# Optimization experiments

Hardware: AMD Instinct MI355X
Metric: run time of the kernel (lower is better)

Reference implementation:

```python
import jax, jax.numpy as jnp
import numpy as np


def setup_inputs() -> dict:
    key = jax.random.key(0)
    k1, k2, k3, k4, k5, k6, k7 = jax.random.split(key, 7)
    B, N, E = 8, 8192, 65536
    Dn, De = 64, 64            # node_shape, edge_shape
    IU = 128                   # input_units
    Dc = 2 * Dn + De           # concat dim = 192
    nodes = jax.random.normal(k1, (B, N, Dn), dtype=jnp.float32)
    edges = jax.random.normal(k2, (B, E, De), dtype=jnp.float32)
    senders = jax.random.randint(k3, (B, E), 0, N, dtype=jnp.int32)
    receivers = jax.random.randint(k4, (B, E), 0, N, dtype=jnp.int32)
    s_in = 1.0 / np.sqrt(Dc)
    s_out = 1.0 / np.sqrt(IU)
    s_edge = 1.0 / np.sqrt(Dn)
    W_in = jax.random.uniform(k5, (Dc, IU), jnp.float32, -s_in, s_in)
    b_in = jnp.zeros((IU,), jnp.float32)
    W_out = jax.random.uniform(k6, (IU, Dn), jnp.float32, -s_out, s_out)
    b_out = jnp.zeros((Dn,), jnp.float32)
    W_edge = jax.random.uniform(k7, (Dn, De), jnp.float32, -s_edge, s_edge)
    b_edge = jnp.zeros((De,), jnp.float32)
    return {"nodes": nodes, "edges": edges, "senders": senders, "receivers": receivers,
            "W_in": W_in, "b_in": b_in, "W_out": W_out, "b_out": b_out,
            "W_edge": W_edge, "b_edge": b_edge}


def reference(nodes, edges, senders, receivers, W_in, b_in, W_out, b_out, W_edge, b_edge):
    B, N, Dn = nodes.shape
    E = edges.shape[1]
    De = edges.shape[2]
    # per-graph offsets so indices address the flattened [B*N] node table
    offsets = (jnp.arange(B, dtype=senders.dtype) * N)[:, None]          # [B,1]
    s_flat = senders.reshape(-1)                                         # [B*E]
    r_flat = receivers.reshape(-1)
    s_off = jnp.where(s_flat != -1, s_flat + jnp.broadcast_to(offsets, (B, E)).reshape(-1), s_flat)
    r_off = jnp.where(r_flat != -1, r_flat + jnp.broadcast_to(offsets, (B, E)).reshape(-1), r_flat)
    nodes_flat = nodes.reshape(B * N, Dn)
    edges_flat = edges.reshape(B * E, De)
    # gather node features onto edges: [recv || edge || send]
    concat = jnp.concatenate([nodes_flat[r_off], edges_flat, nodes_flat[s_off]], axis=1)  # [B*E, 2Dn+De]
    h = jax.nn.relu(concat @ W_in + b_in)            # node_layer_in
    e_new = jax.nn.relu(h @ W_out + b_out)           # node_layer_out -> [B*E, Dn]
    # unsorted_segment_mean over receivers (empty segments -> 0, as in TF)
    sums = jax.ops.segment_sum(e_new, r_off, num_segments=B * N)         # [B*N, Dn]
    counts = jax.ops.segment_sum(jnp.ones((B * E,), e_new.dtype), r_off, num_segments=B * N)
    nodes_new = jnp.where(counts[:, None] > 0, sums / jnp.maximum(counts, 1.0)[:, None], 0.0)
    edges_out = jax.nn.relu(e_new @ W_edge + b_edge)  # edge_layer -> [B*E, De]
    return (nodes_new.reshape(B, N, Dn), edges_out.reshape(B, E, De), s_flat, r_flat)
```

## Files before the change

kernel.cpp:

```cpp
#include <hip/hip_runtime.h>

typedef __attribute__((ext_vector_type(8))) __bf16 bf16x8;
typedef __attribute__((ext_vector_type(4))) __bf16 bf16x4;
typedef __attribute__((ext_vector_type(4))) float f32x4;

constexpr int kB = 8, kN = 8192, kE = 65536;
constexpr int kBN = kB * kN;
constexpr int kBE = kB * kE;
constexpr int kDN = 64, kDE = 64, kIU = 128;

constexpr int XS = 200;
constexpr int HS = 136;
constexpr int ES = 72;

__global__ __launch_bounds__(256, 2)
void edge_mlp_kernel(const float* __restrict__ nodes,
                     const float* __restrict__ edges,
                     const int* __restrict__ senders,
                     const int* __restrict__ receivers,
                     const float* __restrict__ W_in,
                     const float* __restrict__ b_in,
                     const float* __restrict__ W_out,
                     const float* __restrict__ b_out,
                     const float* __restrict__ W_edge,
                     const float* __restrict__ b_edge,
                     float* __restrict__ edges_out,
                     float* __restrict__ sums,
                     float* __restrict__ counts)
{
    __shared__ alignas(16) __bf16 Xs_[64 * XS];
    __shared__ alignas(16) __bf16 Hs_[64 * HS];
    __shared__ alignas(16) __bf16 Es_[64 * ES];
    __shared__ int rgS[64];
    __shared__ int sgS[64];
    __shared__ int rsS[64];

    const int tid  = threadIdx.x;
    const int lane = tid & 63;
    const int wave = tid >> 6;
    const int c16  = lane & 15;
    const int q    = lane >> 4;

    bf16x8 winf[6][2];
#pragma unroll
    for (int kk = 0; kk < 6; ++kk)
#pragma unroll
        for (int nt = 0; nt < 2; ++nt)
#pragma unroll
            for (int j = 0; j < 8; ++j)
                winf[kk][nt][j] =
                    (__bf16)W_in[(kk * 32 + q * 8 + j) * kIU + wave * 32 + nt * 16 + c16];

    bf16x8 woutf[4];
#pragma unroll
    for (int kk = 0; kk < 4; ++kk)
#pragma unroll
        for (int j = 0; j < 8; ++j)
            woutf[kk][j] =
                (__bf16)W_out[(kk * 32 + q * 8 + j) * kDN + wave * 16 + c16];

    bf16x8 wedgef[2];
#pragma unroll
    for (int kk = 0; kk < 2; ++kk)
#pragma unroll
        for (int j = 0; j < 8; ++j)
            wedgef[kk][j] =
                (__bf16)W_edge[(kk * 32 + q * 8 + j) * kDE + wave * 16 + c16];

    const float bin0 = b_in[wave * 32 + c16];
    const float bin1 = b_in[wave * 32 + 16 + c16];
    const float bo   = b_out[wave * 16 + c16];
    const float beg  = b_edge[wave * 16 + c16];

    const int ntiles = kBE / 64;
    for (int t = blockIdx.x; t < ntiles; t += gridDim.x) {
        __syncthreads();
        const int g0 = t * 64;

        if (tid < 64) {
            const int g = g0 + tid;
            const int b = g >> 16;
            const int r = receivers[g];
            const int s = senders[g];
            const int roff = r + (b << 13);
            const int soff = s + (b << 13);
            rgS[tid] = (r < 0) ? (kBN - 1) : roff;
            sgS[tid] = (s < 0) ? (kBN - 1) : soff;
            const int rs = (r < 0) ? -1 : roff;
            rsS[tid] = rs;
            if (rs >= 0) atomicAdd(&counts[rs], 1.0f);
        }
        __syncthreads();

        {
            const int row = tid >> 2;
            const int qt  = tid & 3;
            const float4* nrec = (const float4*)nodes + (size_t)rgS[row] * 16;
            const float4* nsnd = (const float4*)nodes + (size_t)sgS[row] * 16;
            const float4* erow = (const float4*)edges + (size_t)(g0 + row) * 16;
            __bf16* xr = &Xs_[row * XS];
#pragma unroll
            for (int i = 0; i < 4; ++i) {
                const int c = qt * 16 + i * 4;
                float4 a = nrec[qt * 4 + i];
                float4 e = erow[qt * 4 + i];
                float4 s = nsnd[qt * 4 + i];
                bf16x4 pa = {(__bf16)a.x, (__bf16)a.y, (__bf16)a.z, (__bf16)a.w};
                bf16x4 pe = {(__bf16)e.x, (__bf16)e.y, (__bf16)e.z, (__bf16)e.w};
                bf16x4 ps = {(__bf16)s.x, (__bf16)s.y, (__bf16)s.z, (__bf16)s.w};
                *(bf16x4*)&xr[c]       = pa;
                *(bf16x4*)&xr[64 + c]  = pe;
                *(bf16x4*)&xr[128 + c] = ps;
            }
        }
        __syncthreads();

        f32x4 acc1[4][2];
#pragma unroll
        for (int m = 0; m < 4; ++m) {
            acc1[m][0] = (f32x4){0.f, 0.f, 0.f, 0.f};
            acc1[m][1] = (f32x4){0.f, 0.f, 0.f, 0.f};
        }
#pragma unroll
        for (int m = 0; m < 4; ++m) {
            const __bf16* ar = &Xs_[(m * 16 + c16) * XS + q * 8];
            bf16x8 a[6];
#pragma unroll
            for (int kk = 0; kk < 6; ++kk) a[kk] = *(const bf16x8*)(ar + kk * 32);
#pragma unroll
            for (int nt = 0; nt < 2; ++nt)
#pragma unroll
                for (int kk = 0; kk < 6; ++kk)
                    acc1[m][nt] = __builtin_amdgcn_mfma_f32_16x16x32_bf16(
                        a[kk], winf[kk][nt], acc1[m][nt], 0, 0, 0);
        }
#pragma unroll
        for (int m = 0; m < 4; ++m)
#pragma unroll
            for (int nt = 0; nt < 2; ++nt)
#pragma unroll
                for (int r = 0; r < 4; ++r) {
                    float v = acc1[m][nt][r] + (nt ? bin1 : bin0);
                    v = fmaxf(v, 0.f);
                    Hs_[(m * 16 + q * 4 + r) * HS + wave * 32 + nt * 16 + c16] = (__bf16)v;
                }
        __syncthreads();

        f32x4 acc2[4];
#pragma unroll
        for (int m = 0; m < 4; ++m) acc2[m] = (f32x4){0.f, 0.f, 0.f, 0.f};
#pragma unroll
        for (int m = 0; m < 4; ++m) {
            const __bf16* ar = &Hs_[(m * 16 + c16) * HS + q * 8];
            bf16x8 a[4];
#pragma unroll
            for (int kk = 0; kk < 4; ++kk) a[kk] = *(const bf16x8*)(ar + kk * 32);
#pragma unroll
            for (int kk = 0; kk < 4; ++kk)
                acc2[m] = __builtin_amdgcn_mfma_f32_16x16x32_bf16(
                    a[kk], woutf[kk], acc2[m], 0, 0, 0);
        }
#pragma unroll
        for (int m = 0; m < 4; ++m)
#pragma unroll
            for (int r = 0; r < 4; ++r) {
                float v = fmaxf(acc2[m][r] + bo, 0.f);
                Es_[(m * 16 + q * 4 + r) * ES + wave * 16 + c16] = (__bf16)v;
            }
        __syncthreads();

#pragma unroll
        for (int m = 0; m < 4; ++m) {
            const __bf16* ar = &Es_[(m * 16 + c16) * ES + q * 8];
            bf16x8 a0 = *(const bf16x8*)ar;
            bf16x8 a1 = *(const bf16x8*)(ar + 32);
            f32x4 acc3 = (f32x4){0.f, 0.f, 0.f, 0.f};
            acc3 = __builtin_amdgcn_mfma_f32_16x16x32_bf16(a0, wedgef[0], acc3, 0, 0, 0);
            acc3 = __builtin_amdgcn_mfma_f32_16x16x32_bf16(a1, wedgef[1], acc3, 0, 0, 0);
#pragma unroll
            for (int r = 0; r < 4; ++r) {
                float v = fmaxf(acc3[r] + beg, 0.f);
                edges_out[(size_t)(g0 + m * 16 + q * 4 + r) * kDE + wave * 16 + c16] = v;
            }
        }

#pragma unroll
        for (int i = 0; i < 16; ++i) {
            const int row = i * 4 + wave;
            const int rs = rsS[row];
            if (rs >= 0) {
                float v = (float)Es_[row * ES + lane];
                atomicAdd(&sums[(size_t)rs * kDN + lane], v);
            }
        }
    }
}

__global__ __launch_bounds__(256)
void finalize_kernel(const float* __restrict__ sums,
                     const float* __restrict__ counts,
                     const int* __restrict__ senders,
                     const int* __restrict__ receivers,
                     float* __restrict__ out)
{
    constexpr int NQ = kBN * kDN / 4;
    const int t = blockIdx.x * blockDim.x + threadIdx.x;
    if (t < NQ) {
        float4 s = ((const float4*)sums)[t];
        const float c = counts[t >> 4];
        float4 o;
        if (c > 0.f) {
            const float inv = 1.f / c;
            o.x = s.x * inv; o.y = s.y * inv; o.z = s.z * inv; o.w = s.w * inv;
        } else {
            o.x = o.y = o.z = o.w = 0.f;
        }
        ((float4*)out)[t] = o;
    } else {
        const int ci = t - NQ;
        constexpr int base = kBN * kDN + kBE * kDE;
        if (ci < kBE) out[base + ci] = (float)senders[ci];
        else          out[base + ci] = (float)receivers[ci - kBE];
    }
}

extern "C" void kernel_launch(void* const* d_in, const int* in_sizes, int n_in,
                              void* d_out, int out_size, void* d_ws, size_t ws_size,
                              hipStream_t stream) {
    const float* nodes     = (const float*)d_in[0];
    const float* edges     = (const float*)d_in[1];
    const int*   senders   = (const int*)d_in[2];
    const int*   receivers = (const int*)d_in[3];
    const float* W_in      = (const float*)d_in[4];
    const float* b_in      = (const float*)d_in[5];
    const float* W_out     = (const float*)d_in[6];
    const float* b_out     = (const float*)d_in[7];
    const float* W_edge    = (const float*)d_in[8];
    const float* b_edge    = (const float*)d_in[9];

    float* out    = (float*)d_out;
    float* sums   = (float*)d_ws;
    float* counts = sums + (size_t)kBN * kDN;

    hipMemsetAsync(d_ws, 0, (size_t)(kBN * kDN + kBN) * sizeof(float), stream);

    edge_mlp_kernel<<<2048, 256, 0, stream>>>(
        nodes, edges, senders, receivers,
        W_in, b_in, W_out, b_out, W_edge, b_edge,
        out + (size_t)kBN * kDN,
        sums, counts);

    constexpr int total = kBN * kDN / 4 + 2 * kBE;
    finalize_kernel<<<total / 256, 256, 0, stream>>>(
        sums, counts, senders, receivers, out);
}
```

Baseline: 390.5 us.

## Prefetch next tile's gathers into registers and fold index outputs into main kernel

Software-pipelines the edge MLP kernel. The receiver/sender indices and the gathered node and edge rows for the next tile are loaded into registers while the current tile's three MFMA GEMMs run. The separate index-staging phase and the leading __syncthreads are removed, the receiver list is double-buffered in LDS, and plain barriers are replaced by an lgkmcnt-only wait plus s_barrier, so outstanding global loads no longer stall the barrier. The float conversion of senders/receivers moves from the finalize kernel into the main kernel, and the occupancy hint rises to 3 blocks per CU. The 48 extra prefetch registers combined with the higher occupancy target risk register spills.

```diff
diff --git a/kernel.cpp b/kernel.cpp
--- a/kernel.cpp
+++ b/kernel.cpp
@@ -13,7 +13,11 @@
 constexpr int HS = 136;
 constexpr int ES = 72;
 
-__global__ __launch_bounds__(256, 2)
+__device__ __forceinline__ void lds_barrier() {
+    asm volatile("s_waitcnt lgkmcnt(0)\n\ts_barrier" ::: "memory");
+}
+
+__global__ __launch_bounds__(256, 3)
 void edge_mlp_kernel(const float* __restrict__ nodes,
                      const float* __restrict__ edges,
                      const int* __restrict__ senders,
@@ -25,15 +29,15 @@
                      const float* __restrict__ W_edge,
                      const float* __restrict__ b_edge,
                      float* __restrict__ edges_out,
+                     float* __restrict__ out_sf,
+                     float* __restrict__ out_rf,
                      float* __restrict__ sums,
                      float* __restrict__ counts)
 {
     __shared__ alignas(16) __bf16 Xs_[64 * XS];
     __shared__ alignas(16) __bf16 Hs_[64 * HS];
     __shared__ alignas(16) __bf16 Es_[64 * ES];
-    __shared__ int rgS[64];
-    __shared__ int sgS[64];
-    __shared__ int rsS[64];
+    __shared__ int rsS[2][64];
 
     const int tid  = threadIdx.x;
     const int lane = tid & 63;
@@ -72,156 +76,174 @@
     const float bo   = b_out[wave * 16 + c16];
     const float beg  = b_edge[wave * 16 + c16];
 
+    const int row = tid >> 2;
+    const int qt  = tid & 3;
+
     const int ntiles = kBE / 64;
-    for (int t = blockIdx.x; t < ntiles; t += gridDim.x) {
-        __syncthreads();
+    const int stride = gridDim.x;
+
+    int t = blockIdx.x;
+    int rV, sV;
+    int rN, sN;
+    float4 G[12];
+    {
+        const int g = t * 64 + row;
+        rV = receivers[g];
+        sV = senders[g];
+        const int b  = g >> 16;
+        const int rg = (rV < 0) ? (kBN - 1) : rV + (b << 13);
+        const int sg = (sV < 0) ? (kBN - 1) : sV + (b << 13);
+        const float4* nrec = (const float4*)nodes + (size_t)rg * 16;
+        const float4* ez   = (const float4*)edges + (size_t)g * 16;
+        const float4* nsnd = (const float4*)nodes + (size_t)sg * 16;
+#pragma unroll
+        for (int i = 0; i < 4; ++i) {
+            G[i]     = nrec[qt + 4 * i];
+            G[4 + i] = ez  [qt + 4 * i];
+            G[8 + i] = nsnd[qt + 4 * i];
+        }
+        const int t1 = (t + stride < ntiles) ? (t + stride) : t;
+        const int g1 = t1 * 64 + row;
+        rN = receivers[g1];
+        sN = senders[g1];
+    }
+
+    int buf = 0;
+    for (; t < ntiles; t += stride) {
         const int g0 = t * 64;
 
-        if (tid < 64) {
-            const int g = g0 + tid;
-            const int b = g >> 16;
-            const int r = receivers[g];
-            const int s = senders[g];
-            const int roff = r + (b << 13);
-            const int soff = s + (b << 13);
-            rgS[tid] = (r < 0) ? (kBN - 1) : roff;
-            sgS[tid] = (s < 0) ? (kBN - 1) : soff;
-            const int rs = (r < 0) ? -1 : roff;
-            rsS[tid] = rs;
-            if (rs >= 0) atomicAdd(&counts[rs], 1.0f);
-        }
-        __syncthreads();
-
         {
-            const int row = tid >> 2;
-            const int qt  = tid & 3;
-            const float4* nrec = (const float4*)nodes + (size_t)rgS[row] * 16;
-            const float4* nsnd = (const float4*)nodes + (size_t)sgS[row] * 16;
-            const float4* erow = (const float4*)edges + (size_t)(g0 + row) * 16;
+            const int b  = (g0 + row) >> 16;
+            const int rs = (rV < 0) ? -1 : rV + (b << 13);
+            if (qt == 0) {
+                rsS[buf][row] = rs;
+                const int g = g0 + row;
+                out_sf[g] = (float)sV;
+                out_rf[g] = (float)rV;
+                if (rs >= 0) atomicAdd(&counts[rs], 1.0f);
+            }
             __bf16* xr = &Xs_[row * XS];
 #pragma unroll
             for (int i = 0; i < 4; ++i) {
-                const int c = qt * 16 + i * 4;
-                float4 a = nrec[qt * 4 + i];
-                float4 e = erow[qt * 4 + i];
-                float4 s = nsnd[qt * 4 + i];
-                bf16x4 pa = {(__bf16)a.x, (__bf16)a.y, (__bf16)a.z, (__bf16)a.w};
-                bf16x4 pe = {(__bf16)e.x, (__bf16)e.y, (__bf16)e.z, (__bf16)e.w};
-                bf16x4 ps = {(__bf16)s.x, (__bf16)s.y, (__bf16)s.z, (__bf16)s.w};
-                *(bf16x4*)&xr[c]       = pa;
-                *(bf16x4*)&xr[64 + c]  = pe;
-                *(bf16x4*)&xr[128 + c] = ps;
-            }
-        }
-        __syncthreads();
-
-        f32x4 acc1[4][2];
-#pragma unroll
-        for (int m = 0; m < 4; ++m) {
-            acc1[m][0] = (f32x4){0.f, 0.f, 0.f, 0.f};
-            acc1[m][1] = (f32x4){0.f, 0.f, 0.f, 0.f};
-        }
+                const int c = 4 * qt + 16 * i;
+                float4 a = G[i], e = G[4 + i], s = G[8 + i];
+                *(bf16x4*)&xr[c] =
+                    (bf16x4){(__bf16)a.x, (__bf16)a.y, (__bf16)a.z, (__bf16)a.w};
+                *(bf16x4*)&xr[64 + c] =
+                    (bf16x4){(__bf16)e.x, (__bf16)e.y, (__bf16)e.z, (__bf16)e.w};
+                *(bf16x4*)&xr[128 + c] =
+                    (bf16x4){(__bf16)s.x, (__bf16)s.y, (__bf16)s.z, (__bf16)s.w};
+            }
+        }
+        lds_barrier();
+
+        {
+            const int rG = rN, sG = sN;
+            const int tn = (t + stride < ntiles) ? (t + stride) : t;
+            const int gn = tn * 64 + row;
+            const int b  = gn >> 16;
+            const int rg = (rG < 0) ? (kBN - 1) : rG + (b << 13);
+            const int sg = (sG < 0) ? (kBN - 1) : sG + (b << 13);
+            const float4* nrec = (const float4*)nodes + (size_t)rg * 16;
+            const float4* ez   = (const float4*)edges + (size_t)gn * 16;
+            const float4* nsnd = (const float4*)nodes + (size_t)sg * 16;
+#pragma unroll
+            for (int i = 0; i < 4; ++i) {
+                G[i]     = nrec[qt + 4 * i];
+                G[4 + i] = ez  [qt + 4 * i];
+                G[8 + i] = nsnd[qt + 4 * i];
+            }
+            const int t2 = (t + 2 * stride < ntiles) ? (t + 2 * stride) : tn;
+            const int g2 = t2 * 64 + row;
+            rN = receivers[g2];
+            sN = senders[g2];
+            rV = rG;
+            sV = sG;
+        }
+
 #pragma unroll
         for (int m = 0; m < 4; ++m) {
             const __bf16* ar = &Xs_[(m * 16 + c16) * XS + q * 8];
             bf16x8 a[6];
 #pragma unroll
             for (int kk = 0; kk < 6; ++kk) a[kk] = *(const bf16x8*)(ar + kk * 32);
-#pragma unroll
-            for (int nt = 0; nt < 2; ++nt)
-#pragma unroll
-                for (int kk = 0; kk < 6; ++kk)
-                    acc1[m][nt] = __builtin_amdgcn_mfma_f32_16x16x32_bf16(
-                        a[kk], winf[kk][nt], acc1[m][nt], 0, 0, 0);
-        }
-#pragma unroll
-        for (int m = 0; m < 4; ++m)
-#pragma unroll
-            for (int nt = 0; nt < 2; ++nt)
-#pragma unroll
-                for (int r = 0; r < 4; ++r) {
-                    float v = acc1[m][nt][r] + (nt ? bin1 : bin0);
-                    v = fmaxf(v, 0.f);
-                    Hs_[(m * 16 + q * 4 + r) * HS + wave * 32 + nt * 16 + c16] = (__bf16)v;
-                }
-        __syncthreads();
-
-        f32x4 acc2[4];
-#pragma unroll
-        for (int m = 0; m < 4; ++m) acc2[m] = (f32x4){0.f, 0.f, 0.f, 0.f};
+            f32x4 acc0 = (f32x4){0.f, 0.f, 0.f, 0.f};
+            f32x4 acc1 = (f32x4){0.f, 0.f, 0.f, 0.f};
+#pragma unroll
+            for (int kk = 0; kk < 6; ++kk)
+                acc0 = __builtin_amdgcn_mfma_f32_16x16x32_bf16(a[kk], winf[kk][0], acc0, 0, 0, 0);
+#pragma unroll
+            for (int kk = 0; kk < 6; ++kk)
+                acc1 = __builtin_amdgcn_mfma_f32_16x16x32_bf16(a[kk], winf[kk][1], acc1, 0, 0, 0);
+#pragma unroll
+            for (int r = 0; r < 4; ++r) {
+                __bf16* hr = &Hs_[(m * 16 + q * 4 + r) * HS + wave * 32];
+                hr[c16]      = (__bf16)fmaxf(acc0[r] + bin0, 0.f);
+                hr[16 + c16] = (__bf16)fmaxf(acc1[r] + bin1, 0.f);
+            }
+        }
+        lds_barrier();
+
 #pragma unroll
         for (int m = 0; m < 4; ++m) {
             const __bf16* ar = &Hs_[(m * 16 + c16) * HS + q * 8];
             bf16x8 a[4];
 #pragma unroll
             for (int kk = 0; kk < 4; ++kk) a[kk] = *(const bf16x8*)(ar + kk * 32);
+            f32x4 acc = (f32x4){0.f, 0.f, 0.f, 0.f};
 #pragma unroll
             for (int kk = 0; kk < 4; ++kk)
-                acc2[m] = __builtin_amdgcn_mfma_f32_16x16x32_bf16(
-                    a[kk], woutf[kk], acc2[m], 0, 0, 0);
-        }
-#pragma unroll
-        for (int m = 0; m < 4; ++m)
-#pragma unroll
-            for (int r = 0; r < 4; ++r) {
-                float v = fmaxf(acc2[m][r] + bo, 0.f);
-                Es_[(m * 16 + q * 4 + r) * ES + wave * 16 + c16] = (__bf16)v;
-            }
-        __syncthreads();
+                acc = __builtin_amdgcn_mfma_f32_16x16x32_bf16(a[kk], woutf[kk], acc, 0, 0, 0);
+#pragma unroll
+            for (int r = 0; r < 4; ++r)
+                Es_[(m * 16 + q * 4 + r) * ES + wave * 16 + c16] =
+                    (__bf16)fmaxf(acc[r] + bo, 0.f);
+        }
+        lds_barrier();
 
 #pragma unroll
         for (int m = 0; m < 4; ++m) {
             const __bf16* ar = &Es_[(m * 16 + c16) * ES + q * 8];
             bf16x8 a0 = *(const bf16x8*)ar;
             bf16x8 a1 = *(const bf16x8*)(ar + 32);
-            f32x4 acc3 = (f32x4){0.f, 0.f, 0.f, 0.f};
-            acc3 = __builtin_amdgcn_mfma_f32_16x16x32_bf16(a0, wedgef[0], acc3, 0, 0, 0);
-            acc3 = __builtin_amdgcn_mfma_f32_16x16x32_bf16(a1, wedgef[1], acc3, 0, 0, 0);
-#pragma unroll
-            for (int r = 0; r < 4; ++r) {
-                float v = fmaxf(acc3[r] + beg, 0.f);
-                edges_out[(size_t)(g0 + m * 16 + q * 4 + r) * kDE + wave * 16 + c16] = v;
-            }
+            f32x4 acc = (f32x4){0.f, 0.f, 0.f, 0.f};
+            acc = __builtin_amdgcn_mfma_f32_16x16x32_bf16(a0, wedgef[0], acc, 0, 0, 0);
+            acc = __builtin_amdgcn_mfma_f32_16x16x32_bf16(a1, wedgef[1], acc, 0, 0, 0);
+#pragma unroll
+            for (int r = 0; r < 4; ++r)
+                edges_out[(size_t)(g0 + m * 16 + q * 4 + r) * kDE + wave * 16 + c16] =
+                    fmaxf(acc[r] + beg, 0.f);
         }
 
 #pragma unroll
         for (int i = 0; i < 16; ++i) {
-            const int row = i * 4 + wave;
-            const int rs = rsS[row];
+            const int rr = i * 4 + wave;
+            const int rs = rsS[buf][rr];
             if (rs >= 0) {
-                float v = (float)Es_[row * ES + lane];
+                float v = (float)Es_[rr * ES + lane];
                 atomicAdd(&sums[(size_t)rs * kDN + lane], v);
             }
         }
+        buf ^= 1;
     }
 }
 
 __global__ __launch_bounds__(256)
 void finalize_kernel(const float* __restrict__ sums,
                      const float* __restrict__ counts,
-                     const int* __restrict__ senders,
-                     const int* __restrict__ receivers,
                      float* __restrict__ out)
 {
-    constexpr int NQ = kBN * kDN / 4;
     const int t = blockIdx.x * blockDim.x + threadIdx.x;
-    if (t < NQ) {
-        float4 s = ((const float4*)sums)[t];
-        const float c = counts[t >> 4];
-        float4 o;
-        if (c > 0.f) {
-            const float inv = 1.f / c;
-            o.x = s.x * inv; o.y = s.y * inv; o.z = s.z * inv; o.w = s.w * inv;
-        } else {
-            o.x = o.y = o.z = o.w = 0.f;
-        }
-        ((float4*)out)[t] = o;
+    float4 s = ((const float4*)sums)[t];
+    const float c = counts[t >> 4];
+    float4 o;
+    if (c > 0.f) {
+        const float inv = 1.f / c;
+        o.x = s.x * inv; o.y = s.y * inv; o.z = s.z * inv; o.w = s.w * inv;
     } else {
-        const int ci = t - NQ;
-        constexpr int base = kBN * kDN + kBE * kDE;
-        if (ci < kBE) out[base + ci] = (float)senders[ci];
-        else          out[base + ci] = (float)receivers[ci - kBE];
+        o.x = o.y = o.z = o.w = 0.f;
     }
+    ((float4*)out)[t] = o;
 }
 
 extern "C" void kernel_launch(void* const* d_in, const int* in_sizes, int n_in,
@@ -242,15 +264,16 @@
     float* sums   = (float*)d_ws;
     float* counts = sums + (size_t)kBN * kDN;
 
+    float* edges_out = out + (size_t)kBN * kDN;
+    float* out_sf    = edges_out + (size_t)kBE * kDE;
+    float* out_rf    = out_sf + kBE;
+
     hipMemsetAsync(d_ws, 0, (size_t)(kBN * kDN + kBN) * sizeof(float), stream);
 
     edge_mlp_kernel<<<2048, 256, 0, stream>>>(
         nodes, edges, senders, receivers,
         W_in, b_in, W_out, b_out, W_edge, b_edge,
-        out + (size_t)kBN * kDN,
-        sums, counts);
-
-    constexpr int total = kBN * kDN / 4 + 2 * kBE;
-    finalize_kernel<<<total / 256, 256, 0, stream>>>(
-        sums, counts, senders, receivers, out);
-}
+        edges_out, out_sf, out_rf, sums, counts);
+
+    finalize_kernel<<<kBN * kDN / 4 / 256, 256, 0, stream>>>(sums, counts, out);
+}
```

Result: no change. 396.0 us (+1.4%).
